# Optimization experiments

Measured on AMD Instinct MI355X. Metric: run time of the kernel, lower is better.

## Reference

```python
import jax, jax.numpy as jnp
import numpy as np

EPS = 1e-05
QN, QP = -128.0, 127.0


def setup_inputs() -> dict:
    key = jax.random.key(0)
    kx, kw = jax.random.split(key)
    x = jax.random.normal(kx, (4, 2048, 4096), dtype=jnp.float32)
    weight = jax.random.normal(kw, (4096, 4096), dtype=jnp.float32)  # [out, in]
    return {"x": x, "weight": weight}


def reference(x, weight):
    # --- per-token int8 activation quantization (activation_quant) ---
    # s: [B, S, 1], scale so that max(|x|) maps to 127
    s = QP / jnp.clip(jnp.max(jnp.abs(x), axis=-1, keepdims=True), 1e-05, None)
    q = jnp.clip(jnp.round(x * s), QN, QP)  # int8-valued, kept in float
    xq = q / s  # dequantized activations fed to the matmul

    # --- ternary weight quantization (terniarize + pack/unpack round-trip) ---
    scale_w = 1.0 / jnp.clip(jnp.mean(jnp.abs(weight)), EPS, None)
    tw = jnp.clip(jnp.round(weight * scale_w), -1.0, 1.0)  # ternary {-1,0,1}, [out, in]

    # --- bitmat: (xq) @ tw^T, then dequant by weight scale ---
    out = jnp.einsum('bsi,oi->bso', xq, tw) / scale_w
    return out
```

## Files before the change

### kernel.cpp

```cpp
#include <hip/hip_runtime.h>
#include <stdint.h>

#define K_DIM 4096
#define M_TOK 8192
#define N_OUT 4096

typedef int v4i __attribute__((ext_vector_type(4)));


__device__ __forceinline__ void gload_lds16(const void* g, void* l) {
    auto gp = reinterpret_cast<const __attribute__((address_space(1))) uint32_t*>(
        reinterpret_cast<uintptr_t>(g));
    auto lp = reinterpret_cast<__attribute__((address_space(3))) uint32_t*>(
        reinterpret_cast<uintptr_t>(l));
    __builtin_amdgcn_global_load_lds(gp, lp, 16, 0, 0);
}

__global__ void init_acc(double* acc) { *acc = 0.0; }

__global__ __launch_bounds__(256) void quant_act(const float* __restrict__ x,
                                                 int8_t* __restrict__ q,
                                                 float* __restrict__ rs) {
    const int token = blockIdx.x;
    const int t = threadIdx.x;
    const float4* x4 = (const float4*)(x + (size_t)token * K_DIM);
    float4 v[4];
    float m = 0.0f;
#pragma unroll
    for (int r = 0; r < 4; ++r) {
        v[r] = x4[t + 256 * r];
        m = fmaxf(m, fmaxf(fmaxf(fabsf(v[r].x), fabsf(v[r].y)),
                           fmaxf(fabsf(v[r].z), fabsf(v[r].w))));
    }
#pragma unroll
    for (int off = 32; off; off >>= 1) m = fmaxf(m, __shfl_down(m, off, 64));
    __shared__ float wmax[4];
    __shared__ float smax;
    if ((t & 63) == 0) wmax[t >> 6] = m;
    __syncthreads();
    if (t == 0) smax = fmaxf(fmaxf(wmax[0], wmax[1]), fmaxf(wmax[2], wmax[3]));
    __syncthreads();
    const float s = 127.0f / fmaxf(smax, 1e-5f);
    char4* q4 = (char4*)(q + (size_t)token * K_DIM);
#pragma unroll
    for (int r = 0; r < 4; ++r) {
        float4 f = v[r];
        char4 c;
        c.x = (signed char)fminf(fmaxf(rintf(f.x * s), -128.0f), 127.0f);
        c.y = (signed char)fminf(fmaxf(rintf(f.y * s), -128.0f), 127.0f);
        c.z = (signed char)fminf(fmaxf(rintf(f.z * s), -128.0f), 127.0f);
        c.w = (signed char)fminf(fmaxf(rintf(f.w * s), -128.0f), 127.0f);
        q4[t + 256 * r] = c;
    }
    if (t == 0) rs[token] = 1.0f / s;
}

__global__ __launch_bounds__(256) void wabs_sum(const float* __restrict__ w,
                                                double* __restrict__ acc) {
    const size_t n4 = (size_t)N_OUT * K_DIM / 4;
    const size_t stride = (size_t)gridDim.x * 256;
    const float4* w4 = (const float4*)w;
    float sum = 0.0f;
    for (size_t j = (size_t)blockIdx.x * 256 + threadIdx.x; j < n4; j += stride) {
        float4 f = w4[j];
        sum += fabsf(f.x) + fabsf(f.y) + fabsf(f.z) + fabsf(f.w);
    }
    double d = (double)sum;
#pragma unroll
    for (int off = 32; off; off >>= 1) d += __shfl_down(d, off, 64);
    __shared__ double wsum[4];
    const int t = threadIdx.x;
    if ((t & 63) == 0) wsum[t >> 6] = d;
    __syncthreads();
    if (t == 0) atomicAdd(acc, wsum[0] + wsum[1] + wsum[2] + wsum[3]);
}

__global__ __launch_bounds__(256) void ternarize(const float* __restrict__ w,
                                                 int8_t* __restrict__ tw,
                                                 const double* __restrict__ acc) {
    const double mean = *acc * (1.0 / ((double)N_OUT * (double)K_DIM));
    const float sw = 1.0f / fmaxf((float)mean, 1e-5f);
    const size_t i = (size_t)blockIdx.x * 256 + threadIdx.x;
    const float4* w4 = (const float4*)w;
    char4* t4 = (char4*)tw;
    float4 f = w4[i];
    char4 c;
    c.x = (signed char)fminf(fmaxf(rintf(f.x * sw), -1.0f), 1.0f);
    c.y = (signed char)fminf(fmaxf(rintf(f.y * sw), -1.0f), 1.0f);
    c.z = (signed char)fminf(fmaxf(rintf(f.z * sw), -1.0f), 1.0f);
    c.w = (signed char)fminf(fmaxf(rintf(f.w * sw), -1.0f), 1.0f);
    t4[i] = c;
}

__global__ __launch_bounds__(256) void gemm_i8(const int8_t* __restrict__ A,
                                               const int8_t* __restrict__ B,
                                               const float* __restrict__ rs,
                                               const double* __restrict__ acc,
                                               float* __restrict__ out) {
    const int bm = blockIdx.y * 128;
    const int bn = blockIdx.x * 128;
    __shared__ int8_t As[128 * 64];
    __shared__ int8_t Bs[128 * 64];
    const int t = threadIdx.x;
    const int lane = t & 63;
    const int wave = t >> 6;
    const int wm = (wave >> 1) * 64;
    const int wn = (wave & 1) * 64;

    v4i accv[4][4] = {};

    const int srow = t >> 2;
    const int scol = (t & 3) * 16;
    const int8_t* Ag = A + (size_t)(bm + srow) * K_DIM + scol;
    const int8_t* Bg = B + (size_t)(bn + srow) * K_DIM + scol;
    int8_t* lA0 = As + t * 16;
    int8_t* lA1 = As + 4096 + t * 16;
    int8_t* lB0 = Bs + t * 16;
    int8_t* lB1 = Bs + 4096 + t * 16;

    const int kb = (lane >> 4) * 16;
    const int fr = lane & 15;

    for (int k0 = 0; k0 < K_DIM; k0 += 64) {
        gload_lds16(Ag + k0, lA0);
        gload_lds16(Ag + (size_t)64 * K_DIM + k0, lA1);
        gload_lds16(Bg + k0, lB0);
        gload_lds16(Bg + (size_t)64 * K_DIM + k0, lB1);
        __syncthreads();

        v4i af[4], bf[4];
#pragma unroll
        for (int i = 0; i < 4; ++i)
            af[i] = *(const v4i*)(As + (wm + i * 16 + fr) * 64 + kb);
#pragma unroll
        for (int j = 0; j < 4; ++j)
            bf[j] = *(const v4i*)(Bs + (wn + j * 16 + fr) * 64 + kb);
#pragma unroll
        for (int i = 0; i < 4; ++i)
#pragma unroll
            for (int j = 0; j < 4; ++j)
                accv[i][j] = __builtin_amdgcn_mfma_i32_16x16x64_i8(af[i], bf[j], accv[i][j], 0, 0, 0);
        __syncthreads();
    }

    const double mean = *acc * (1.0 / ((double)N_OUT * (double)K_DIM));
    const float wmean = fmaxf((float)mean, 1e-5f);
    const int crow0 = (lane >> 4) * 4;
    const int ccol = lane & 15;
#pragma unroll
    for (int i = 0; i < 4; ++i) {
        const int rbase = bm + wm + i * 16 + crow0;
#pragma unroll
        for (int reg = 0; reg < 4; ++reg) {
            const int r = rbase + reg;
            const float scale = rs[r] * wmean;
            float* orow = out + (size_t)r * N_OUT + bn + wn + ccol;
#pragma unroll
            for (int j = 0; j < 4; ++j)
                orow[j * 16] = (float)accv[i][j][reg] * scale;
        }
    }
}

extern "C" void kernel_launch(void* const* d_in, const int* in_sizes, int n_in,
                              void* d_out, int out_size, void* d_ws, size_t ws_size,
                              hipStream_t stream) {
    const float* x = (const float*)d_in[0];
    const float* w = (const float*)d_in[1];
    float* out = (float*)d_out;
    char* ws = (char*)d_ws;
    int8_t* q = (int8_t*)ws;
    int8_t* tw = (int8_t*)(ws + 33554432);
    float* rs = (float*)(ws + 50331648);
    double* acc = (double*)(ws + 50364416);

    hipLaunchKernelGGL(init_acc, dim3(1), dim3(1), 0, stream, acc);
    hipLaunchKernelGGL(quant_act, dim3(M_TOK), dim3(256), 0, stream, x, q, rs);
    hipLaunchKernelGGL(wabs_sum, dim3(1024), dim3(256), 0, stream, w, acc);
    hipLaunchKernelGGL(ternarize, dim3((N_OUT * (size_t)K_DIM / 4) / 256), dim3(256), 0, stream, w, tw, acc);
    hipLaunchKernelGGL(gemm_i8, dim3(N_OUT / 128, M_TOK / 128), dim3(256), 0, stream, q, tw, rs, acc, out);
}
```

Measured before the change: 431.1 us.

## Enlarge GEMM tile to 256x256 with 8 waves and swizzled LDS layout

The int8 GEMM block tile grows from 128x128 to 256x256 with 512 threads, each wave covering 64x128 outputs, which raises data reuse per LDS load. LDS columns are XOR-swizzled on both the global-to-LDS store and the fragment reads to cut bank conflicts. The accumulator init kernel is folded into quant_act, and wabs_sum gets a larger grid. The bigger tile raises register pressure (32 accumulators per lane) and halves the number of blocks, which may lower occupancy.

Result: slower. 441.6 us (+2.4%).

```diff
diff --git a/kernel.cpp b/kernel.cpp
--- a/kernel.cpp
+++ b/kernel.cpp
@@ -16,13 +16,13 @@
     __builtin_amdgcn_global_load_lds(gp, lp, 16, 0, 0);
 }
 
-__global__ void init_acc(double* acc) { *acc = 0.0; }
-
 __global__ __launch_bounds__(256) void quant_act(const float* __restrict__ x,
                                                  int8_t* __restrict__ q,
-                                                 float* __restrict__ rs) {
+                                                 float* __restrict__ rs,
+                                                 double* __restrict__ acc) {
     const int token = blockIdx.x;
     const int t = threadIdx.x;
+    if (token == 0 && t == 0) *acc = 0.0;
     const float4* x4 = (const float4*)(x + (size_t)token * K_DIM);
     float4 v[4];
     float m = 0.0f;
@@ -92,53 +92,55 @@
     t4[i] = c;
 }
 
-__global__ __launch_bounds__(256) void gemm_i8(const int8_t* __restrict__ A,
+__global__ __launch_bounds__(512) void gemm_i8(const int8_t* __restrict__ A,
                                                const int8_t* __restrict__ B,
                                                const float* __restrict__ rs,
                                                const double* __restrict__ acc,
                                                float* __restrict__ out) {
-    const int bm = blockIdx.y * 128;
-    const int bn = blockIdx.x * 128;
-    __shared__ int8_t As[128 * 64];
-    __shared__ int8_t Bs[128 * 64];
+    const int bm = blockIdx.y * 256;
+    const int bn = blockIdx.x * 256;
+    __shared__ int8_t As[256 * 64];
+    __shared__ int8_t Bs[256 * 64];
     const int t = threadIdx.x;
     const int lane = t & 63;
     const int wave = t >> 6;
     const int wm = (wave >> 1) * 64;
-    const int wn = (wave & 1) * 64;
+    const int wn = (wave & 1) * 128;
 
-    v4i accv[4][4] = {};
+    v4i accv[4][8] = {};
 
     const int srow = t >> 2;
-    const int scol = (t & 3) * 16;
-    const int8_t* Ag = A + (size_t)(bm + srow) * K_DIM + scol;
-    const int8_t* Bg = B + (size_t)(bn + srow) * K_DIM + scol;
+    const int scol = (((t & 3) ^ ((t >> 3) & 3)) << 4);
+    const int8_t* Ag0 = A + (size_t)(bm + srow) * K_DIM + scol;
+    const int8_t* Ag1 = Ag0 + (size_t)128 * K_DIM;
+    const int8_t* Bg0 = B + (size_t)(bn + srow) * K_DIM + scol;
+    const int8_t* Bg1 = Bg0 + (size_t)128 * K_DIM;
     int8_t* lA0 = As + t * 16;
-    int8_t* lA1 = As + 4096 + t * 16;
+    int8_t* lA1 = As + 8192 + t * 16;
     int8_t* lB0 = Bs + t * 16;
-    int8_t* lB1 = Bs + 4096 + t * 16;
+    int8_t* lB1 = Bs + 8192 + t * 16;
 
-    const int kb = (lane >> 4) * 16;
     const int fr = lane & 15;
+    const int sw16 = (((lane >> 4) ^ ((fr >> 1) & 3)) << 4);
 
     for (int k0 = 0; k0 < K_DIM; k0 += 64) {
-        gload_lds16(Ag + k0, lA0);
-        gload_lds16(Ag + (size_t)64 * K_DIM + k0, lA1);
-        gload_lds16(Bg + k0, lB0);
-        gload_lds16(Bg + (size_t)64 * K_DIM + k0, lB1);
+        gload_lds16(Ag0 + k0, lA0);
+        gload_lds16(Ag1 + k0, lA1);
+        gload_lds16(Bg0 + k0, lB0);
+        gload_lds16(Bg1 + k0, lB1);
         __syncthreads();
 
-        v4i af[4], bf[4];
+        v4i af[4], bf[8];
 #pragma unroll
         for (int i = 0; i < 4; ++i)
-            af[i] = *(const v4i*)(As + (wm + i * 16 + fr) * 64 + kb);
+            af[i] = *(const v4i*)(As + (wm + i * 16 + fr) * 64 + sw16);
 #pragma unroll
-        for (int j = 0; j < 4; ++j)
-            bf[j] = *(const v4i*)(Bs + (wn + j * 16 + fr) * 64 + kb);
+        for (int j = 0; j < 8; ++j)
+            bf[j] = *(const v4i*)(Bs + (wn + j * 16 + fr) * 64 + sw16);
 #pragma unroll
         for (int i = 0; i < 4; ++i)
 #pragma unroll
-            for (int j = 0; j < 4; ++j)
+            for (int j = 0; j < 8; ++j)
                 accv[i][j] = __builtin_amdgcn_mfma_i32_16x16x64_i8(af[i], bf[j], accv[i][j], 0, 0, 0);
         __syncthreads();
     }
@@ -156,7 +158,7 @@
             const float scale = rs[r] * wmean;
             float* orow = out + (size_t)r * N_OUT + bn + wn + ccol;
 #pragma unroll
-            for (int j = 0; j < 4; ++j)
+            for (int j = 0; j < 8; ++j)
                 orow[j * 16] = (float)accv[i][j][reg] * scale;
         }
     }
@@ -174,9 +176,8 @@
     float* rs = (float*)(ws + 50331648);
     double* acc = (double*)(ws + 50364416);
 
-    hipLaunchKernelGGL(init_acc, dim3(1), dim3(1), 0, stream, acc);
-    hipLaunchKernelGGL(quant_act, dim3(M_TOK), dim3(256), 0, stream, x, q, rs);
-    hipLaunchKernelGGL(wabs_sum, dim3(1024), dim3(256), 0, stream, w, acc);
+    hipLaunchKernelGGL(quant_act, dim3(M_TOK), dim3(256), 0, stream, x, q, rs, acc);
+    hipLaunchKernelGGL(wabs_sum, dim3(2048), dim3(256), 0, stream, w, acc);
     hipLaunchKernelGGL(ternarize, dim3((N_OUT * (size_t)K_DIM / 4) / 256), dim3(256), 0, stream, w, tw, acc);
-    hipLaunchKernelGGL(gemm_i8, dim3(N_OUT / 128, M_TOK / 128), dim3(256), 0, stream, q, tw, rs, acc, out);
+    hipLaunchKernelGGL(gemm_i8, dim3(N_OUT / 256, M_TOK / 256), dim3(512), 0, stream, q, tw, rs, acc, out);
 }
```
